# Kernel tuning notes

Measured on AMD Instinct MI355X. Metric: run time of the kernel, lower is better.

Reference implementation:

```python
import jax, jax.numpy as jnp
import numpy as np

Q = 2.0
TEMPERATURE = 1.0
EXP = 1.0 / (Q - 1.0)  # exponent 1/(q-1); q=2 -> sparsemax-style projection
N_BISECT_ITERS = 50    # enough for xtol ~ 1e-6 over an interval of width ~ (u_max - u_min + 10)


def setup_inputs() -> dict:
    key = jax.random.key(0)
    k_x, k_w1, k_w2 = jax.random.split(key, 3)
    B, D, H, E = 8192, 4096, 256, 64
    x = jax.random.normal(k_x, (B, D), dtype=jnp.float32)
    w1 = jax.random.normal(k_w1, (D, H), dtype=jnp.float32) * 0.02
    b1 = jnp.zeros((H,), dtype=jnp.float32)
    w2 = jax.random.normal(k_w2, (H, E), dtype=jnp.float32) * 0.05
    b2 = jnp.zeros((E,), dtype=jnp.float32)
    return {"x": x, "w1": w1, "b1": b1, "w2": w2, "b2": b2}


def _bisect_tau(us):
    # us: [B, E] = utilities / temperature. Find per-row tau with sum(relu(us - tau)**EXP) = 1.
    lo = jnp.min(us, axis=-1) - 10.0   # constraint(lo) > 0
    hi = jnp.max(us, axis=-1)          # constraint(hi) = -1 < 0

    def body(i, carry):
        lo, hi = carry
        mid = 0.5 * (lo + hi)
        f = jnp.sum(jnp.maximum(us - mid[..., None], 0.0) ** EXP, axis=-1) - 1.0
        pos = f > 0.0  # constraint is decreasing in tau: root is above mid
        return (jnp.where(pos, mid, lo), jnp.where(pos, hi, mid))

    lo, hi = jax.lax.fori_loop(0, N_BISECT_ITERS, body, (lo, hi))
    return 0.5 * (lo + hi)  # [B]


def reference(x, w1, b1, w2, b2):
    # utility_net (Dropout is identity in eval mode)
    h = jax.nn.relu(x @ w1 + b1)            # [B, 256]
    utilities = h @ w2 + b2                  # [B, E]
    us = utilities / TEMPERATURE
    # tau is found by root-finding on detached values in the original (.item()),
    # so it is a constant w.r.t. differentiation.
    tau = jax.lax.stop_gradient(_bisect_tau(jax.lax.stop_gradient(us)))
    p = jnp.maximum(us - tau[..., None], 0.0) ** EXP   # [B, E]
    p = p / (jnp.sum(p, axis=-1, keepdims=True) + 1e-8)
    return p
```

## Files before the change

### kernel.cpp

```cpp
#include <hip/hip_runtime.h>
#include <stdint.h>

typedef _Float16 f16;
typedef _Float16 f16x8 __attribute__((ext_vector_type(8)));
typedef _Float16 f16x4 __attribute__((ext_vector_type(4)));
typedef float f32x4 __attribute__((ext_vector_type(4)));

#define D_DIM 4096
#define H_DIM 256
#define E_DIM 64
#define BM 32
#define BK 64
#define NKT (D_DIM / BK)

__global__ void pack_w1_kernel(const float* __restrict__ w1, f16* __restrict__ w1s) {
  const int u = blockIdx.x * blockDim.x + threadIdx.x;
  const int lane = u & 63;
  const int kk = (u >> 6) & 1;
  const int c16 = (u >> 7) & 15;
  const int kt = u >> 11;
  const int g = lane >> 4, r = lane & 15;
  const int k0 = kt * 64 + kk * 32 + g * 8;
  const int col = c16 * 16 + r;
  f16x8 o;
#pragma unroll
  for (int j = 0; j < 8; ++j) o[j] = (f16)w1[(size_t)(k0 + j) * H_DIM + col];
  *(f16x8*)(w1s + (size_t)u * 8) = o;
}

__global__ void pack_w2_kernel(const float* __restrict__ w2, f16* __restrict__ w2s) {
  const int u = blockIdx.x * blockDim.x + threadIdx.x;
  const int lane = u & 63;
  const int ks = (u >> 6) & 7;
  const int cg = u >> 9;
  const int g = lane >> 4, r = lane & 15;
  const int k0 = ks * 32 + g * 8;
  const int col = cg * 16 + r;
  f16x8 o;
#pragma unroll
  for (int j = 0; j < 8; ++j) o[j] = (f16)w2[(size_t)(k0 + j) * E_DIM + col];
  *(f16x8*)(w2s + (size_t)u * 8) = o;
}

__launch_bounds__(512)
__global__ void fused_kernel(const float* __restrict__ x,
                             const f16* __restrict__ w1s,
                             const float* __restrict__ b1,
                             const f16* __restrict__ w2s,
                             const float* __restrict__ b2,
                             float* __restrict__ out) {
  __shared__ __align__(16) char smem[24576];
  f16* As0 = (f16*)smem;
  f16* As1 = (f16*)(smem + 4096);
  f16* h_lds = (f16*)smem;
  float* u_lds = (float*)(smem + 16384);

  const int t = threadIdx.x;
  const int lane = t & 63;
  const int wn = t >> 6;
  const int g = lane >> 4, r = lane & 15;
  const int brow = blockIdx.x * BM;

  const int a_row = t >> 4;
  const int a_col = (t & 15) << 2;
  const int a_sw = a_col ^ ((a_row & 7) << 3);
  const float* xrow = x + (size_t)(brow + a_row) * D_DIM + a_col;

  const f16* bptr = w1s + (size_t)(wn * 2) * 1024 + lane * 8;

  f32x4 acc[2][2] = {{{0.f,0.f,0.f,0.f},{0.f,0.f,0.f,0.f}},
                     {{0.f,0.f,0.f,0.f},{0.f,0.f,0.f,0.f}}};
  f16x8 B0[4], B1[4];
  float4 xE, xO;

#define LDX(kt) (*(const float4*)(xrow + (kt) * 64))
#define LDB(kt, B)                                                  \
  {                                                                 \
    const f16* p_ = bptr + (size_t)(kt) * 16384;                    \
    B[0] = *(const f16x8*)(p_);                        \
    B[1] = *(const f16x8*)(p_ + 512);                  \
    B[2] = *(const f16x8*)(p_ + 1024);                 \
    B[3] = *(const f16x8*)(p_ + 1536);                 \
  }
#define STW(As, v)                                                  \
  {                                                                 \
    f16x4 hv_;                                                      \
    hv_[0] = (f16)(v).x; hv_[1] = (f16)(v).y;                       \
    hv_[2] = (f16)(v).z; hv_[3] = (f16)(v).w;                       \
    *(f16x4*)((As) + a_row * 64 + a_sw) = hv_;                      \
  }
#define COMP(As, B)                                                            \
  {                                                                            \
    _Pragma("unroll") for (int kk = 0; kk < 2; ++kk) {                         \
      const int kb_ = kk * 32 + g * 8;                                         \
      _Pragma("unroll") for (int rh = 0; rh < 2; ++rh) {                       \
        const int arow_ = rh * 16 + r;                                         \
        const f16x8 af_ =                                                      \
            *(const f16x8*)((As) + arow_ * 64 + (kb_ ^ ((arow_ & 7) << 3)));   \
        _Pragma("unroll") for (int ch = 0; ch < 2; ++ch) {                     \
          acc[rh][ch] = __builtin_amdgcn_mfma_f32_16x16x32_f16(                \
              af_, B[kk + ch * 2], acc[rh][ch], 0, 0, 0);                      \
        }                                                                      \
      }                                                                        \
    }                                                                          \
  }
#define BAR()                                          \
  asm volatile("s_waitcnt lgkmcnt(0)" ::: "memory");   \
  __builtin_amdgcn_s_barrier();

  {
    float4 t0 = LDX(0);
    LDB(0, B0);
    LDB(1, B1);
    xE = LDX(1);
    xO = LDX(2);
    STW(As0, t0);
    BAR();
  }

#pragma unroll 1
  for (int s = 0; s < NKT; s += 2) {
    STW(As1, xE);
    xE = LDX(s + 3 < NKT ? s + 3 : NKT - 1);
    COMP(As0, B0);
    LDB(s + 2 < NKT ? s + 2 : NKT - 1, B0);
    BAR();
    STW(As0, xO);
    xO = LDX(s + 4 < NKT ? s + 4 : NKT - 1);
    COMP(As1, B1);
    LDB(s + 3 < NKT ? s + 3 : NKT - 1, B1);
    BAR();
  }

#pragma unroll
  for (int rh = 0; rh < 2; ++rh)
#pragma unroll
    for (int ch = 0; ch < 2; ++ch) {
      const int col = wn * 32 + ch * 16 + r;
      const float bias = b1[col];
#pragma unroll
      for (int j = 0; j < 4; ++j) {
        const int row = rh * 16 + g * 4 + j;
        float v = acc[rh][ch][j] + bias;
        v = fmaxf(v, 0.f);
        h_lds[row * 256 + (col ^ ((row & 7) << 3))] = (f16)v;
      }
    }
  __syncthreads();

  const int rh2 = wn & 1;
  const int cg = wn >> 1;
  f32x4 acc2 = {0.f, 0.f, 0.f, 0.f};
  const f16* w2p = w2s + (size_t)(cg * 8) * 512 + lane * 8;
#pragma unroll
  for (int ks = 0; ks < 8; ++ks) {
    const int arow = rh2 * 16 + r;
    const int kb = ks * 32 + g * 8;
    const f16x8 af = *(const f16x8*)(h_lds + arow * 256 + (kb ^ ((arow & 7) << 3)));
    const f16x8 bf = *(const f16x8*)(w2p + ks * 512);
    acc2 = __builtin_amdgcn_mfma_f32_16x16x32_f16(af, bf, acc2, 0, 0, 0);
  }
  {
    const int col = cg * 16 + r;
    const float bias = b2[col];
#pragma unroll
    for (int j = 0; j < 4; ++j) {
      const int row = rh2 * 16 + g * 4 + j;
      u_lds[row * 64 + col] = acc2[j] + bias;
    }
  }
  __syncthreads();

  const int srow = wn * 4 + (lane >> 4);
  const int scol = (lane & 15) << 2;
  const float4 uv = *(const float4*)(u_lds + srow * 64 + scol);
  float u0 = uv.x, u1 = uv.y, u2 = uv.z, u3 = uv.w;

  float mx = fmaxf(fmaxf(u0, u1), fmaxf(u2, u3));
  float mn = fminf(fminf(u0, u1), fminf(u2, u3));
#pragma unroll
  for (int m = 1; m < 16; m <<= 1) {
    mx = fmaxf(mx, __shfl_xor(mx, m));
    mn = fminf(mn, __shfl_xor(mn, m));
  }
  float lo = mn - 10.0f, hi = mx;
#pragma unroll 1
  for (int it = 0; it < 32; ++it) {
    const float mid = 0.5f * (lo + hi);
    float s = fmaxf(u0 - mid, 0.f) + fmaxf(u1 - mid, 0.f) +
              fmaxf(u2 - mid, 0.f) + fmaxf(u3 - mid, 0.f);
#pragma unroll
    for (int m = 1; m < 16; m <<= 1) s += __shfl_xor(s, m);
    const bool pos = (s - 1.0f) > 0.0f;
    lo = pos ? mid : lo;
    hi = pos ? hi : mid;
  }
  const float tau = 0.5f * (lo + hi);
  const float p0 = fmaxf(u0 - tau, 0.f);
  const float p1 = fmaxf(u1 - tau, 0.f);
  const float p2 = fmaxf(u2 - tau, 0.f);
  const float p3 = fmaxf(u3 - tau, 0.f);
  float sum = p0 + p1 + p2 + p3;
#pragma unroll
  for (int m = 1; m < 16; m <<= 1) sum += __shfl_xor(sum, m);
  const float inv = 1.0f / (sum + 1e-8f);
  float4 pv;
  pv.x = p0 * inv; pv.y = p1 * inv; pv.z = p2 * inv; pv.w = p3 * inv;
  *(float4*)(out + (size_t)(brow + srow) * E_DIM + scol) = pv;
}

extern "C" void kernel_launch(void* const* d_in, const int* in_sizes, int n_in,
                              void* d_out, int out_size, void* d_ws, size_t ws_size,
                              hipStream_t stream) {
  const float* x  = (const float*)d_in[0];
  const float* w1 = (const float*)d_in[1];
  const float* b1 = (const float*)d_in[2];
  const float* w2 = (const float*)d_in[3];
  const float* b2 = (const float*)d_in[4];
  float* out = (float*)d_out;

  char* wsb = (char*)d_ws;
  f16* w1s = (f16*)wsb;
  f16* w2s = (f16*)(wsb + (2u << 20));

  pack_w1_kernel<<<512, 256, 0, stream>>>(w1, w1s);
  pack_w2_kernel<<<8, 256, 0, stream>>>(w2, w2s);
  fused_kernel<<<8192 / BM, 512, 0, stream>>>(x, w1s, b1, w2s, b2, out);
}
```

Before: 55.03 us.

## Deepen GEMM pipeline to four LDS stages and merge weight pack kernels

```diff
diff --git a/kernel.cpp b/kernel.cpp
--- a/kernel.cpp
+++ b/kernel.cpp
@@ -11,35 +11,38 @@
 #define E_DIM 64
 #define BM 32
 #define BK 64
-#define NKT (D_DIM / BK)
-
-__global__ void pack_w1_kernel(const float* __restrict__ w1, f16* __restrict__ w1s) {
-  const int u = blockIdx.x * blockDim.x + threadIdx.x;
-  const int lane = u & 63;
-  const int kk = (u >> 6) & 1;
-  const int c16 = (u >> 7) & 15;
-  const int kt = u >> 11;
-  const int g = lane >> 4, r = lane & 15;
-  const int k0 = kt * 64 + kk * 32 + g * 8;
-  const int col = c16 * 16 + r;
-  f16x8 o;
-#pragma unroll
-  for (int j = 0; j < 8; ++j) o[j] = (f16)w1[(size_t)(k0 + j) * H_DIM + col];
-  *(f16x8*)(w1s + (size_t)u * 8) = o;
-}
-
-__global__ void pack_w2_kernel(const float* __restrict__ w2, f16* __restrict__ w2s) {
-  const int u = blockIdx.x * blockDim.x + threadIdx.x;
-  const int lane = u & 63;
-  const int ks = (u >> 6) & 7;
-  const int cg = u >> 9;
-  const int g = lane >> 4, r = lane & 15;
-  const int k0 = ks * 32 + g * 8;
-  const int col = cg * 16 + r;
-  f16x8 o;
-#pragma unroll
-  for (int j = 0; j < 8; ++j) o[j] = (f16)w2[(size_t)(k0 + j) * E_DIM + col];
-  *(f16x8*)(w2s + (size_t)u * 8) = o;
+#define NKT 64
+
+__global__ void pack_kernel(const float* __restrict__ w1, f16* __restrict__ w1s,
+                            const float* __restrict__ w2, f16* __restrict__ w2s) {
+  const int b = blockIdx.x;
+  const int t = threadIdx.x;
+  if (b < 512) {
+    const int u = b * 256 + t;
+    const int lane = u & 63;
+    const int kk = (u >> 6) & 1;
+    const int c16 = (u >> 7) & 15;
+    const int kt = u >> 11;
+    const int g = lane >> 4, r = lane & 15;
+    const int k0 = kt * 64 + kk * 32 + g * 8;
+    const int col = c16 * 16 + r;
+    f16x8 o;
+#pragma unroll
+    for (int j = 0; j < 8; ++j) o[j] = (f16)w1[(size_t)(k0 + j) * H_DIM + col];
+    *(f16x8*)(w1s + (size_t)u * 8) = o;
+  } else {
+    const int u = (b - 512) * 256 + t;
+    const int lane = u & 63;
+    const int ks = (u >> 6) & 7;
+    const int cg = u >> 9;
+    const int g = lane >> 4, r = lane & 15;
+    const int k0 = ks * 32 + g * 8;
+    const int col = cg * 16 + r;
+    f16x8 o;
+#pragma unroll
+    for (int j = 0; j < 8; ++j) o[j] = (f16)w2[(size_t)(k0 + j) * E_DIM + col];
+    *(f16x8*)(w2s + (size_t)u * 8) = o;
+  }
 }
 
 __launch_bounds__(512)
@@ -50,8 +53,7 @@
                              const float* __restrict__ b2,
                              float* __restrict__ out) {
   __shared__ __align__(16) char smem[24576];
-  f16* As0 = (f16*)smem;
-  f16* As1 = (f16*)(smem + 4096);
+  f16* As = (f16*)smem;
   f16* h_lds = (f16*)smem;
   float* u_lds = (float*)(smem + 16384);
 
@@ -65,41 +67,40 @@
   const int a_col = (t & 15) << 2;
   const int a_sw = a_col ^ ((a_row & 7) << 3);
   const float* xrow = x + (size_t)(brow + a_row) * D_DIM + a_col;
-
   const f16* bptr = w1s + (size_t)(wn * 2) * 1024 + lane * 8;
 
   f32x4 acc[2][2] = {{{0.f,0.f,0.f,0.f},{0.f,0.f,0.f,0.f}},
                      {{0.f,0.f,0.f,0.f},{0.f,0.f,0.f,0.f}}};
-  f16x8 B0[4], B1[4];
-  float4 xE, xO;
-
-#define LDX(kt) (*(const float4*)(xrow + (kt) * 64))
+  f16x8 BA[8], BB[8];
+  float4 xA[2], xB[2];
+
+#define LDX(kt) (*(const float4*)(xrow + (size_t)(kt) * 64))
 #define LDB(kt, B)                                                  \
   {                                                                 \
     const f16* p_ = bptr + (size_t)(kt) * 16384;                    \
-    B[0] = *(const f16x8*)(p_);                        \
-    B[1] = *(const f16x8*)(p_ + 512);                  \
-    B[2] = *(const f16x8*)(p_ + 1024);                 \
-    B[3] = *(const f16x8*)(p_ + 1536);                 \
-  }
-#define STW(As, v)                                                  \
+    (B)[0] = *(const f16x8*)(p_);                                   \
+    (B)[1] = *(const f16x8*)(p_ + 512);                             \
+    (B)[2] = *(const f16x8*)(p_ + 1024);                            \
+    (B)[3] = *(const f16x8*)(p_ + 1536);                            \
+  }
+#define STW(dst, v)                                                 \
   {                                                                 \
     f16x4 hv_;                                                      \
     hv_[0] = (f16)(v).x; hv_[1] = (f16)(v).y;                       \
     hv_[2] = (f16)(v).z; hv_[3] = (f16)(v).w;                       \
-    *(f16x4*)((As) + a_row * 64 + a_sw) = hv_;                      \
-  }
-#define COMP(As, B)                                                            \
+    *(f16x4*)((dst) + a_row * 64 + a_sw) = hv_;                     \
+  }
+#define COMP(Ab, B)                                                            \
   {                                                                            \
     _Pragma("unroll") for (int kk = 0; kk < 2; ++kk) {                         \
       const int kb_ = kk * 32 + g * 8;                                         \
       _Pragma("unroll") for (int rh = 0; rh < 2; ++rh) {                       \
         const int arow_ = rh * 16 + r;                                         \
         const f16x8 af_ =                                                      \
-            *(const f16x8*)((As) + arow_ * 64 + (kb_ ^ ((arow_ & 7) << 3)));   \
+            *(const f16x8*)((Ab) + arow_ * 64 + (kb_ ^ ((arow_ & 7) << 3)));   \
         _Pragma("unroll") for (int ch = 0; ch < 2; ++ch) {                     \
           acc[rh][ch] = __builtin_amdgcn_mfma_f32_16x16x32_f16(                \
-              af_, B[kk + ch * 2], acc[rh][ch], 0, 0, 0);                      \
+              af_, (B)[kk + ch * 2], acc[rh][ch], 0, 0, 0);                    \
         }                                                                      \
       }                                                                        \
     }                                                                          \
@@ -108,28 +109,41 @@
   asm volatile("s_waitcnt lgkmcnt(0)" ::: "memory");   \
   __builtin_amdgcn_s_barrier();
 
+#define PHASE(s0, Bc, Bn, xc)                                     \
+  {                                                               \
+    STW(As + (((s0) + 2) & 3) * 2048, (xc)[0]);                   \
+    STW(As + (((s0) + 3) & 3) * 2048, (xc)[1]);                   \
+    {                                                             \
+      int sx0 = (s0) + 6; if (sx0 > 63) sx0 = 63;                 \
+      int sx1 = (s0) + 7; if (sx1 > 63) sx1 = 63;                 \
+      (xc)[0] = LDX(sx0); (xc)[1] = LDX(sx1);                     \
+    }                                                             \
+    {                                                             \
+      int sb0 = (s0) + 2; if (sb0 > 63) sb0 = 63;                 \
+      int sb1 = (s0) + 3; if (sb1 > 63) sb1 = 63;                 \
+      LDB(sb0, Bn); LDB(sb1, (Bn) + 4);                           \
+    }                                                             \
+    COMP(As + ((s0) & 3) * 2048, Bc);                             \
+    COMP(As + (((s0) + 1) & 3) * 2048, (Bc) + 4);                 \
+    BAR();                                                        \
+  }
+
   {
     float4 t0 = LDX(0);
-    LDB(0, B0);
-    LDB(1, B1);
-    xE = LDX(1);
-    xO = LDX(2);
-    STW(As0, t0);
+    float4 t1 = LDX(1);
+    LDB(0, BA); LDB(1, BA + 4);
+    xA[0] = LDX(2); xA[1] = LDX(3);
+    xB[0] = LDX(4); xB[1] = LDX(5);
+    STW(As, t0);
+    STW(As + 2048, t1);
     BAR();
   }
 
 #pragma unroll 1
-  for (int s = 0; s < NKT; s += 2) {
-    STW(As1, xE);
-    xE = LDX(s + 3 < NKT ? s + 3 : NKT - 1);
-    COMP(As0, B0);
-    LDB(s + 2 < NKT ? s + 2 : NKT - 1, B0);
-    BAR();
-    STW(As0, xO);
-    xO = LDX(s + 4 < NKT ? s + 4 : NKT - 1);
-    COMP(As1, B1);
-    LDB(s + 3 < NKT ? s + 3 : NKT - 1, B1);
-    BAR();
+  for (int pp = 0; pp < 16; ++pp) {
+    const int s0 = pp * 4;
+    PHASE(s0, BA, BB, xA);
+    PHASE(s0 + 2, BB, BA, xB);
   }
 
 #pragma unroll
@@ -223,7 +237,6 @@
   f16* w1s = (f16*)wsb;
   f16* w2s = (f16*)(wsb + (2u << 20));
 
-  pack_w1_kernel<<<512, 256, 0, stream>>>(w1, w1s);
-  pack_w2_kernel<<<8, 256, 0, stream>>>(w2, w2s);
+  pack_kernel<<<520, 256, 0, stream>>>(w1, w1s, w2, w2s);
   fused_kernel<<<8192 / BM, 512, 0, stream>>>(x, w1s, b1, w2s, b2, out);
 }
```

Result: no change. 54.44 us (-1.1%).

## Split first GEMM over K into four partial kernels plus reduce-fused epilogue

Applied to the files above, without the earlier changes.

```diff
diff --git a/kernel.cpp b/kernel.cpp
--- a/kernel.cpp
+++ b/kernel.cpp
@@ -11,62 +11,62 @@
 #define E_DIM 64
 #define BM 32
 #define BK 64
-#define NKT (D_DIM / BK)
-
-__global__ void pack_w1_kernel(const float* __restrict__ w1, f16* __restrict__ w1s) {
-  const int u = blockIdx.x * blockDim.x + threadIdx.x;
-  const int lane = u & 63;
-  const int kk = (u >> 6) & 1;
-  const int c16 = (u >> 7) & 15;
-  const int kt = u >> 11;
-  const int g = lane >> 4, r = lane & 15;
-  const int k0 = kt * 64 + kk * 32 + g * 8;
-  const int col = c16 * 16 + r;
-  f16x8 o;
-#pragma unroll
-  for (int j = 0; j < 8; ++j) o[j] = (f16)w1[(size_t)(k0 + j) * H_DIM + col];
-  *(f16x8*)(w1s + (size_t)u * 8) = o;
-}
-
-__global__ void pack_w2_kernel(const float* __restrict__ w2, f16* __restrict__ w2s) {
-  const int u = blockIdx.x * blockDim.x + threadIdx.x;
-  const int lane = u & 63;
-  const int ks = (u >> 6) & 7;
-  const int cg = u >> 9;
-  const int g = lane >> 4, r = lane & 15;
-  const int k0 = ks * 32 + g * 8;
-  const int col = cg * 16 + r;
-  f16x8 o;
-#pragma unroll
-  for (int j = 0; j < 8; ++j) o[j] = (f16)w2[(size_t)(k0 + j) * E_DIM + col];
-  *(f16x8*)(w2s + (size_t)u * 8) = o;
+#define KSPLIT 4
+#define NKT2 16
+
+__global__ void pack_kernel(const float* __restrict__ w1, f16* __restrict__ w1s,
+                            const float* __restrict__ w2, f16* __restrict__ w2s) {
+  const int b = blockIdx.x;
+  const int t = threadIdx.x;
+  if (b < 512) {
+    const int u = b * 256 + t;
+    const int lane = u & 63;
+    const int kk = (u >> 6) & 1;
+    const int c16 = (u >> 7) & 15;
+    const int kt = u >> 11;
+    const int g = lane >> 4, r = lane & 15;
+    const int k0 = kt * 64 + kk * 32 + g * 8;
+    const int col = c16 * 16 + r;
+    f16x8 o;
+#pragma unroll
+    for (int j = 0; j < 8; ++j) o[j] = (f16)w1[(size_t)(k0 + j) * H_DIM + col];
+    *(f16x8*)(w1s + (size_t)u * 8) = o;
+  } else {
+    const int u = (b - 512) * 256 + t;
+    const int lane = u & 63;
+    const int ks = (u >> 6) & 7;
+    const int cg = u >> 9;
+    const int g = lane >> 4, r = lane & 15;
+    const int k0 = ks * 32 + g * 8;
+    const int col = cg * 16 + r;
+    f16x8 o;
+#pragma unroll
+    for (int j = 0; j < 8; ++j) o[j] = (f16)w2[(size_t)(k0 + j) * E_DIM + col];
+    *(f16x8*)(w2s + (size_t)u * 8) = o;
+  }
 }
 
 __launch_bounds__(512)
-__global__ void fused_kernel(const float* __restrict__ x,
-                             const f16* __restrict__ w1s,
-                             const float* __restrict__ b1,
-                             const f16* __restrict__ w2s,
-                             const float* __restrict__ b2,
-                             float* __restrict__ out) {
-  __shared__ __align__(16) char smem[24576];
-  f16* As0 = (f16*)smem;
-  f16* As1 = (f16*)(smem + 4096);
-  f16* h_lds = (f16*)smem;
-  float* u_lds = (float*)(smem + 16384);
+__global__ void gemm1_splitk_kernel(const float* __restrict__ x,
+                                    const f16* __restrict__ w1s,
+                                    float* __restrict__ hpart) {
+  __shared__ __align__(16) f16 As0[BM * BK];
+  __shared__ __align__(16) f16 As1[BM * BK];
 
   const int t = threadIdx.x;
   const int lane = t & 63;
   const int wn = t >> 6;
   const int g = lane >> 4, r = lane & 15;
-  const int brow = blockIdx.x * BM;
+  const int bid = blockIdx.x;
+  const int ks = bid & 3;
+  const int rb = bid >> 2;
+  const int brow = rb * BM;
 
   const int a_row = t >> 4;
   const int a_col = (t & 15) << 2;
   const int a_sw = a_col ^ ((a_row & 7) << 3);
-  const float* xrow = x + (size_t)(brow + a_row) * D_DIM + a_col;
-
-  const f16* bptr = w1s + (size_t)(wn * 2) * 1024 + lane * 8;
+  const float* xrow = x + (size_t)(brow + a_row) * D_DIM + ks * 1024 + a_col;
+  const f16* bptr = w1s + (size_t)ks * 16 * 16384 + (size_t)(wn * 2) * 1024 + lane * 8;
 
   f32x4 acc[2][2] = {{{0.f,0.f,0.f,0.f},{0.f,0.f,0.f,0.f}},
                      {{0.f,0.f,0.f,0.f},{0.f,0.f,0.f,0.f}}};
@@ -77,10 +77,10 @@
 #define LDB(kt, B)                                                  \
   {                                                                 \
     const f16* p_ = bptr + (size_t)(kt) * 16384;                    \
-    B[0] = *(const f16x8*)(p_);                        \
-    B[1] = *(const f16x8*)(p_ + 512);                  \
-    B[2] = *(const f16x8*)(p_ + 1024);                 \
-    B[3] = *(const f16x8*)(p_ + 1536);                 \
+    (B)[0] = *(const f16x8*)(p_);                                   \
+    (B)[1] = *(const f16x8*)(p_ + 512);                             \
+    (B)[2] = *(const f16x8*)(p_ + 1024);                            \
+    (B)[3] = *(const f16x8*)(p_ + 1536);                            \
   }
 #define STW(As, v)                                                  \
   {                                                                 \
@@ -99,7 +99,7 @@
             *(const f16x8*)((As) + arow_ * 64 + (kb_ ^ ((arow_ & 7) << 3)));   \
         _Pragma("unroll") for (int ch = 0; ch < 2; ++ch) {                     \
           acc[rh][ch] = __builtin_amdgcn_mfma_f32_16x16x32_f16(                \
-              af_, B[kk + ch * 2], acc[rh][ch], 0, 0, 0);                      \
+              af_, (B)[kk + ch * 2], acc[rh][ch], 0, 0, 0);                    \
         }                                                                      \
       }                                                                        \
     }                                                                          \
@@ -119,33 +119,76 @@
   }
 
 #pragma unroll 1
-  for (int s = 0; s < NKT; s += 2) {
+  for (int s = 0; s < NKT2; s += 2) {
     STW(As1, xE);
-    xE = LDX(s + 3 < NKT ? s + 3 : NKT - 1);
+    xE = LDX(s + 3 < NKT2 ? s + 3 : NKT2 - 1);
     COMP(As0, B0);
-    LDB(s + 2 < NKT ? s + 2 : NKT - 1, B0);
+    LDB(s + 2 < NKT2 ? s + 2 : NKT2 - 1, B0);
     BAR();
     STW(As0, xO);
-    xO = LDX(s + 4 < NKT ? s + 4 : NKT - 1);
+    xO = LDX(s + 4 < NKT2 ? s + 4 : NKT2 - 1);
     COMP(As1, B1);
-    LDB(s + 3 < NKT ? s + 3 : NKT - 1, B1);
+    LDB(s + 3 < NKT2 ? s + 3 : NKT2 - 1, B1);
     BAR();
   }
 
+  float* hp = hpart + (size_t)bid * (BM * H_DIM);
 #pragma unroll
   for (int rh = 0; rh < 2; ++rh)
 #pragma unroll
     for (int ch = 0; ch < 2; ++ch) {
       const int col = wn * 32 + ch * 16 + r;
-      const float bias = b1[col];
 #pragma unroll
       for (int j = 0; j < 4; ++j) {
         const int row = rh * 16 + g * 4 + j;
-        float v = acc[rh][ch][j] + bias;
-        v = fmaxf(v, 0.f);
-        h_lds[row * 256 + (col ^ ((row & 7) << 3))] = (f16)v;
+        hp[row * H_DIM + col] = acc[rh][ch][j];
       }
     }
+}
+
+__launch_bounds__(512)
+__global__ void reduce_fused_kernel(const float* __restrict__ hpart,
+                                    const float* __restrict__ b1,
+                                    const f16* __restrict__ w2s,
+                                    const float* __restrict__ b2,
+                                    float* __restrict__ out) {
+  __shared__ __align__(16) char smem[24576];
+  f16* h_lds = (f16*)smem;
+  float* u_lds = (float*)(smem + 16384);
+
+  const int t = threadIdx.x;
+  const int lane = t & 63;
+  const int wn = t >> 6;
+  const int g = lane >> 4, r = lane & 15;
+  const int brow = blockIdx.x * BM;
+
+  const float* base = hpart + (size_t)blockIdx.x * (KSPLIT * BM * H_DIM);
+  float4 s[4];
+#pragma unroll
+  for (int i = 0; i < 4; ++i)
+    s[i] = *(const float4*)(base + (size_t)(i * 512 + t) * 4);
+#pragma unroll
+  for (int c = 1; c < KSPLIT; ++c) {
+    const float* cb = base + (size_t)c * (BM * H_DIM);
+#pragma unroll
+    for (int i = 0; i < 4; ++i) {
+      const float4 v = *(const float4*)(cb + (size_t)(i * 512 + t) * 4);
+      s[i].x += v.x; s[i].y += v.y; s[i].z += v.z; s[i].w += v.w;
+    }
+  }
+#pragma unroll
+  for (int i = 0; i < 4; ++i) {
+    const int f = i * 512 + t;
+    const int row = f >> 6;
+    const int col = (f & 63) << 2;
+    const float4 bv = *(const float4*)(b1 + col);
+    f16x4 hv;
+    hv[0] = (f16)fmaxf(s[i].x + bv.x, 0.f);
+    hv[1] = (f16)fmaxf(s[i].y + bv.y, 0.f);
+    hv[2] = (f16)fmaxf(s[i].z + bv.z, 0.f);
+    hv[3] = (f16)fmaxf(s[i].w + bv.w, 0.f);
+    *(f16x4*)(h_lds + row * 256 + (col ^ ((row & 7) << 3))) = hv;
+  }
   __syncthreads();
 
   const int rh2 = wn & 1;
@@ -153,11 +196,11 @@
   f32x4 acc2 = {0.f, 0.f, 0.f, 0.f};
   const f16* w2p = w2s + (size_t)(cg * 8) * 512 + lane * 8;
 #pragma unroll
-  for (int ks = 0; ks < 8; ++ks) {
+  for (int ksi = 0; ksi < 8; ++ksi) {
     const int arow = rh2 * 16 + r;
-    const int kb = ks * 32 + g * 8;
+    const int kb = ksi * 32 + g * 8;
     const f16x8 af = *(const f16x8*)(h_lds + arow * 256 + (kb ^ ((arow & 7) << 3)));
-    const f16x8 bf = *(const f16x8*)(w2p + ks * 512);
+    const f16x8 bf = *(const f16x8*)(w2p + ksi * 512);
     acc2 = __builtin_amdgcn_mfma_f32_16x16x32_f16(af, bf, acc2, 0, 0, 0);
   }
   {
@@ -187,11 +230,11 @@
 #pragma unroll 1
   for (int it = 0; it < 32; ++it) {
     const float mid = 0.5f * (lo + hi);
-    float s = fmaxf(u0 - mid, 0.f) + fmaxf(u1 - mid, 0.f) +
-              fmaxf(u2 - mid, 0.f) + fmaxf(u3 - mid, 0.f);
-#pragma unroll
-    for (int m = 1; m < 16; m <<= 1) s += __shfl_xor(s, m);
-    const bool pos = (s - 1.0f) > 0.0f;
+    float sm = fmaxf(u0 - mid, 0.f) + fmaxf(u1 - mid, 0.f) +
+               fmaxf(u2 - mid, 0.f) + fmaxf(u3 - mid, 0.f);
+#pragma unroll
+    for (int m = 1; m < 16; m <<= 1) sm += __shfl_xor(sm, m);
+    const bool pos = (sm - 1.0f) > 0.0f;
     lo = pos ? mid : lo;
     hi = pos ? hi : mid;
   }
@@ -222,8 +265,9 @@
   char* wsb = (char*)d_ws;
   f16* w1s = (f16*)wsb;
   f16* w2s = (f16*)(wsb + (2u << 20));
-
-  pack_w1_kernel<<<512, 256, 0, stream>>>(w1, w1s);
-  pack_w2_kernel<<<8, 256, 0, stream>>>(w2, w2s);
-  fused_kernel<<<8192 / BM, 512, 0, stream>>>(x, w1s, b1, w2s, b2, out);
-}
+  float* hpart = (float*)(wsb + (4u << 20));
+
+  pack_kernel<<<520, 256, 0, stream>>>(w1, w1s, w2, w2s);
+  gemm1_splitk_kernel<<<1024, 512, 0, stream>>>(x, w1s, hpart);
+  reduce_fused_kernel<<<256, 512, 0, stream>>>(hpart, b1, w2s, b2, out);
+}
```

New measurement: 60.25 us. 1.09x slower.
